# Performance work log

Measured on AMD Instinct MI355X. Metric: run time of the kernel, lower is better.

Reference implementation:

```python
import jax, jax.numpy as jnp
import numpy as np

H = 16  # num_heads (from init_kwargs)


def setup_inputs() -> dict:
    key = jax.random.key(0)
    ks = jax.random.split(key, 12)
    B, S, E = 4, 1024, 1024
    inp = {
        "query": jax.random.normal(ks[0], (B, S, E), jnp.float32),
        "key": jax.random.normal(ks[1], (B, S, E), jnp.float32),
        "value": jax.random.normal(ks[2], (B, S, E), jnp.float32),
        "mask": jax.random.randint(ks[3], (B, S, S), 0, 2, jnp.int32),
        # nn.Linear params: y = x @ W.T + b
        "Wq": jax.random.normal(ks[4], (E, E), jnp.float32) * 0.02,
        "bq": jnp.zeros((E,), jnp.float32),
        "Wk": jax.random.normal(ks[5], (E, E), jnp.float32) * 0.02,
        "bk": jnp.zeros((E,), jnp.float32),
        "Wv": jax.random.normal(ks[6], (E, E), jnp.float32) * 0.02,
        "bv": jnp.zeros((E,), jnp.float32),
        "Wo": jax.random.normal(ks[7], (E, E), jnp.float32) * 0.02,
        "bo": jnp.zeros((E,), jnp.float32),
    }
    return inp


def reference(query, key, value, mask, Wq, bq, Wk, bk, Wv, bv, Wo, bo):
    # Dropout treated as identity (eval mode) for a deterministic baseline.
    B, Sq, E = query.shape
    Sk = key.shape[1]
    D = E // H
    scale = jnp.sqrt(jnp.float32(D))

    Q = (query @ Wq.T + bq).reshape(B, Sq, H, D).transpose(0, 2, 1, 3)  # bhqd
    K = (key @ Wk.T + bk).reshape(B, Sk, H, D).transpose(0, 2, 1, 3)    # bhkd
    V = (value @ Wv.T + bv).reshape(B, Sk, H, D).transpose(0, 2, 1, 3)  # bhkd

    scores = jnp.einsum("bhqd,bhkd->bhqk", Q, K) / scale
    scores = jnp.where(mask[:, None, :, :] == 0, jnp.float32(-1e9), scores)
    attn = jax.nn.softmax(scores, axis=-1)  # [B,H,Sq,Sk]

    ctx = jnp.einsum("bhqk,bhkd->bhqd", attn, V)
    ctx = ctx.transpose(0, 2, 1, 3).reshape(B, Sq, E)
    out = ctx @ Wo.T + bo
    attn_avg = attn.mean(axis=1)  # [B,Sq,Sk]
    return out, attn_avg
```

## Files before the change

kernel.cpp:

```cpp
#include <hip/hip_runtime.h>
#include <hip/hip_bf16.h>
#include <stdint.h>

#define BATCH 4
#define SEQ   1024
#define EMB   1024
#define NH    16
#define HD    64

typedef short s8v __attribute__((ext_vector_type(8)));
typedef float f4v __attribute__((ext_vector_type(4)));

__device__ __forceinline__ uint16_t f2bf(float f) {
    __hip_bfloat16 h = __float2bfloat16(f);
    return *reinterpret_cast<uint16_t*>(&h);
}
__device__ __forceinline__ short bfraw(float f) {
    __hip_bfloat16 h = __float2bfloat16(f);
    return *reinterpret_cast<short*>(&h);
}
__device__ __forceinline__ s8v cvt8(const float* p) {
    float4 a = *(const float4*)p;
    float4 b = *(const float4*)(p + 4);
    s8v r;
    r[0] = bfraw(a.x); r[1] = bfraw(a.y); r[2] = bfraw(a.z); r[3] = bfraw(a.w);
    r[4] = bfraw(b.x); r[5] = bfraw(b.y); r[6] = bfraw(b.z); r[7] = bfraw(b.w);
    return r;
}

__global__ __launch_bounds__(256) void pack_mask(
        const int* __restrict__ mask, unsigned long long* __restrict__ Mb64)
{
    const size_t gid = (size_t)blockIdx.x * 256 + threadIdx.x;
    const unsigned long long bal = __ballot(mask[gid] != 0);
    if ((threadIdx.x & 63) == 0) Mb64[gid >> 6] = bal;
}

__global__ __launch_bounds__(256) void cvt_all(
        const float* __restrict__ W0, const float* __restrict__ W1,
        const float* __restrict__ W2, const float* __restrict__ W3,
        const float* __restrict__ X0, const float* __restrict__ X1,
        const float* __restrict__ X2,
        uint16_t* __restrict__ Wdst, uint16_t* __restrict__ Xq,
        uint16_t* __restrict__ Xk, uint16_t* __restrict__ Xv)
{
    const int y = blockIdx.y;
    const size_t off = ((size_t)blockIdx.x * 256 + threadIdx.x) * 8;
    if (y < 4) {
        if (blockIdx.x >= 512) return;
        const float* s = (y == 0) ? W0 : (y == 1) ? W1 : (y == 2) ? W2 : W3;
        *(s8v*)(Wdst + (size_t)y * EMB * EMB + off) = cvt8(s + off);
    } else {
        const float* s = (y == 4) ? X0 : (y == 5) ? X1 : X2;
        uint16_t*    d = (y == 4) ? Xq : (y == 5) ? Xk : Xv;
        *(s8v*)(d + off) = cvt8(s + off);
    }
}

__global__ __launch_bounds__(512, 2) void gemm3(
        const uint16_t* __restrict__ X0, const uint16_t* __restrict__ W0,
        const float* __restrict__ b0, void* __restrict__ o0, int sc0, float ss0,
        const uint16_t* __restrict__ X1, const uint16_t* __restrict__ W1,
        const float* __restrict__ b1, void* __restrict__ o1, int sc1, float ss1,
        const uint16_t* __restrict__ X2, const uint16_t* __restrict__ W2,
        const float* __restrict__ b2, void* __restrict__ o2, int sc2, float ss2)
{
    __shared__ __attribute__((aligned(16))) uint16_t As[2][128][40];
    __shared__ __attribute__((aligned(16))) uint16_t Bs[2][128][40];

    const int z = blockIdx.z;
    const uint16_t* Xb   = (z == 0) ? X0 : (z == 1) ? X1 : X2;
    const uint16_t* Wb   = (z == 0) ? W0 : (z == 1) ? W1 : W2;
    const float*    bias = (z == 0) ? b0 : (z == 1) ? b1 : b2;
    void*           outv = (z == 0) ? o0 : (z == 1) ? o1 : o2;
    const int     scatter = (z == 0) ? sc0 : (z == 1) ? sc1 : sc2;
    const float   scale   = (z == 0) ? ss0 : (z == 1) ? ss1 : ss2;

    const int t    = threadIdx.x;
    const int lane = t & 63;
    const int w    = t >> 6;
    const int wm = w & 1;
    const int wn = w >> 1;
    const int m0 = blockIdx.y * 128;
    const int n0 = blockIdx.x * 128;
    const int ar = lane & 15;
    const int aq = lane >> 4;

    const int srow = t >> 2;
    const int scol = (t & 3) * 8;

    const uint16_t* gA = Xb + (size_t)(m0 + srow) * EMB + scol;
    const uint16_t* gB = Wb + (size_t)(n0 + srow) * EMB + scol;

    f4v acc[4][2];
    #pragma unroll
    for (int i = 0; i < 4; ++i)
        #pragma unroll
        for (int j = 0; j < 2; ++j) acc[i][j] = (f4v){0.f, 0.f, 0.f, 0.f};

    s8v ra = *(const s8v*)gA;
    s8v rb = *(const s8v*)gB;

    for (int ki = 0; ki < 32; ++ki) {
        const int cur = ki & 1;
        *(s8v*)&As[cur][srow][scol] = ra;
        *(s8v*)&Bs[cur][srow][scol] = rb;
        __syncthreads();

        if (ki + 1 < 32) {
            const int kn = (ki + 1) * 32;
            ra = *(const s8v*)(gA + kn);
            rb = *(const s8v*)(gB + kn);
        }
        __builtin_amdgcn_sched_barrier(0);

        s8v af[4], bf[2];
        #pragma unroll
        for (int i = 0; i < 4; ++i)
            af[i] = *(const s8v*)&As[cur][wm * 64 + i * 16 + ar][aq * 8];
        #pragma unroll
        for (int j = 0; j < 2; ++j)
            bf[j] = *(const s8v*)&Bs[cur][wn * 32 + j * 16 + ar][aq * 8];
        #pragma unroll
        for (int i = 0; i < 4; ++i)
            #pragma unroll
            for (int j = 0; j < 2; ++j)
                acc[i][j] = __builtin_amdgcn_mfma_f32_16x16x32_bf16(af[i], bf[j], acc[i][j], 0, 0, 0);
    }

    #pragma unroll
    for (int i = 0; i < 4; ++i) {
        const int crow = m0 + wm * 64 + i * 16 + aq * 4;
        #pragma unroll
        for (int j = 0; j < 2; ++j) {
            const int n = n0 + wn * 32 + j * 16 + ar;
            const float bv = bias[n];
            #pragma unroll
            for (int r = 0; r < 4; ++r) {
                const int m = crow + r;
                const float v = (acc[i][j][r] + bv) * scale;
                if (scatter == 1) {
                    size_t idx = (size_t)(((m >> 10) * NH + (n >> 6)) * SEQ + (m & 1023)) * HD + (n & 63);
                    ((uint16_t*)outv)[idx] = f2bf(v);
                } else if (scatter == 2) {
                    size_t idx = (size_t)(((m >> 10) * NH + (n >> 6)) * HD + (n & 63)) * SEQ + (m & 1023);
                    ((uint16_t*)outv)[idx] = f2bf(v);
                } else {
                    ((float*)outv)[(size_t)m * EMB + n] = v;
                }
            }
        }
    }
}

__global__ __launch_bounds__(256, 4) void flash_ctx(
        const uint16_t* __restrict__ Qb, const uint16_t* __restrict__ Kb,
        const uint16_t* __restrict__ Vt, const uint32_t* __restrict__ Mb,
        uint16_t* __restrict__ ctx, float* __restrict__ linv_out)
{
    __shared__ uint32_t Ml[4][16][33];
    __shared__ __attribute__((aligned(16))) uint16_t Pt[4][2][16][56];

    const int t = threadIdx.x;
    const int w = t >> 6, lane = t & 63;
    const int ar = lane & 15, aq = lane >> 4;

    const int id   = blockIdx.x;
    const int xcd  = id & 7;
    const int rest = id >> 3;
    const int bh   = xcd * 8 + (rest & 7);
    const int qt   = (rest >> 3) * 4 + w;
    const int b = bh >> 4, h = bh & 15;
    const size_t hb = ((size_t)(b * NH + h)) * SEQ * HD;

    {
        const uint32_t* src = Mb + (((size_t)b * SEQ + qt * 16) << 5);
        uint4 m0 = *(const uint4*)(src + lane * 8);
        uint4 m1 = *(const uint4*)(src + lane * 8 + 4);
        const int pr = (lane * 8) >> 5, pc = (lane * 8) & 31;
        Ml[w][pr][pc + 0] = m0.x; Ml[w][pr][pc + 1] = m0.y;
        Ml[w][pr][pc + 2] = m0.z; Ml[w][pr][pc + 3] = m0.w;
        Ml[w][pr][pc + 4] = m1.x; Ml[w][pr][pc + 5] = m1.y;
        Ml[w][pr][pc + 6] = m1.z; Ml[w][pr][pc + 7] = m1.w;
    }

    const uint16_t* qp = Qb + hb + (size_t)(qt * 16 + ar) * HD + aq * 8;
    const s8v a0 = *(const s8v*)qp;
    const s8v a1 = *(const s8v*)(qp + 32);

    const uint16_t* kbase = Kb + hb + (size_t)ar * HD + aq * 8;
    const uint16_t* vbase = Vt + hb + (size_t)ar * SEQ + aq * 8;

    f4v OA0 = {0.f,0.f,0.f,0.f}, OA1 = OA0, OA2 = OA0, OA3 = OA0;
    f4v OB0 = OA0, OB1 = OA0, OB2 = OA0, OB3 = OA0;
    float lsA[4] = {0.f, 0.f, 0.f, 0.f};
    float lsB[4] = {0.f, 0.f, 0.f, 0.f};

    for (int ci = 0; ci < 16; ++ci) {
        const int cA = ci * 2, cB = ci * 2 + 1;
        const int kcA = cA * 32, kcB = cB * 32;

        const uint16_t* kA = kbase + (size_t)kcA * HD;
        const uint16_t* kB = kbase + (size_t)kcB * HD;
        s8v Abl0 = *(const s8v*)kA,            Abh0 = *(const s8v*)(kA + 32);
        s8v Abl1 = *(const s8v*)(kA + 16*HD),  Abh1 = *(const s8v*)(kA + 16*HD + 32);
        s8v Bbl0 = *(const s8v*)kB,            Bbh0 = *(const s8v*)(kB + 32);
        s8v Bbl1 = *(const s8v*)(kB + 16*HD),  Bbh1 = *(const s8v*)(kB + 16*HD + 32);

        f4v z = {0.f,0.f,0.f,0.f};
        f4v sA0 = __builtin_amdgcn_mfma_f32_16x16x32_bf16(a0, Abl0, z, 0, 0, 0);
        sA0 = __builtin_amdgcn_mfma_f32_16x16x32_bf16(a1, Abh0, sA0, 0, 0, 0);
        f4v sA1 = __builtin_amdgcn_mfma_f32_16x16x32_bf16(a0, Abl1, z, 0, 0, 0);
        sA1 = __builtin_amdgcn_mfma_f32_16x16x32_bf16(a1, Abh1, sA1, 0, 0, 0);
        f4v sB0 = __builtin_amdgcn_mfma_f32_16x16x32_bf16(a0, Bbl0, z, 0, 0, 0);
        sB0 = __builtin_amdgcn_mfma_f32_16x16x32_bf16(a1, Bbh0, sB0, 0, 0, 0);
        f4v sB1 = __builtin_amdgcn_mfma_f32_16x16x32_bf16(a0, Bbl1, z, 0, 0, 0);
        sB1 = __builtin_amdgcn_mfma_f32_16x16x32_bf16(a1, Bbh1, sB1, 0, 0, 0);

        const uint16_t* vA = vbase + kcA;
        const uint16_t* vB = vbase + kcB;
        s8v Av0 = *(const s8v*)(vA);
        s8v Av1 = *(const s8v*)(vA + 16 * SEQ);
        s8v Av2 = *(const s8v*)(vA + 32 * SEQ);
        s8v Av3 = *(const s8v*)(vA + 48 * SEQ);
        s8v Bv0 = *(const s8v*)(vB);
        s8v Bv1 = *(const s8v*)(vB + 16 * SEQ);
        s8v Bv2 = *(const s8v*)(vB + 32 * SEQ);
        s8v Bv3 = *(const s8v*)(vB + 48 * SEQ);

        #pragma unroll
        for (int r = 0; r < 4; ++r) {
            const uint32_t mwA = Ml[w][aq * 4 + r][cA];
            const float e0 = ((mwA >> ar) & 1u)        ? __expf(sA0[r]) : 0.f;
            const float e1 = ((mwA >> (16 + ar)) & 1u) ? __expf(sA1[r]) : 0.f;
            lsA[r] += e0 + e1;
            Pt[w][0][aq * 4 + r][ar]      = f2bf(e0);
            Pt[w][0][aq * 4 + r][16 + ar] = f2bf(e1);
        }
        #pragma unroll
        for (int r = 0; r < 4; ++r) {
            const uint32_t mwB = Ml[w][aq * 4 + r][cB];
            const float e0 = ((mwB >> ar) & 1u)        ? __expf(sB0[r]) : 0.f;
            const float e1 = ((mwB >> (16 + ar)) & 1u) ? __expf(sB1[r]) : 0.f;
            lsB[r] += e0 + e1;
            Pt[w][1][aq * 4 + r][ar]      = f2bf(e0);
            Pt[w][1][aq * 4 + r][16 + ar] = f2bf(e1);
        }

        const s8v paA = *(const s8v*)&Pt[w][0][ar][aq * 8];
        OA0 = __builtin_amdgcn_mfma_f32_16x16x32_bf16(paA, Av0, OA0, 0, 0, 0);
        OA1 = __builtin_amdgcn_mfma_f32_16x16x32_bf16(paA, Av1, OA1, 0, 0, 0);
        OA2 = __builtin_amdgcn_mfma_f32_16x16x32_bf16(paA, Av2, OA2, 0, 0, 0);
        OA3 = __builtin_amdgcn_mfma_f32_16x16x32_bf16(paA, Av3, OA3, 0, 0, 0);
        const s8v paB = *(const s8v*)&Pt[w][1][ar][aq * 8];
        OB0 = __builtin_amdgcn_mfma_f32_16x16x32_bf16(paB, Bv0, OB0, 0, 0, 0);
        OB1 = __builtin_amdgcn_mfma_f32_16x16x32_bf16(paB, Bv1, OB1, 0, 0, 0);
        OB2 = __builtin_amdgcn_mfma_f32_16x16x32_bf16(paB, Bv2, OB2, 0, 0, 0);
        OB3 = __builtin_amdgcn_mfma_f32_16x16x32_bf16(paB, Bv3, OB3, 0, 0, 0);
    }

    float lsum[4];
    #pragma unroll
    for (int r = 0; r < 4; ++r) {
        OA0[r] += OB0[r]; OA1[r] += OB1[r];
        OA2[r] += OB2[r]; OA3[r] += OB3[r];
        lsum[r] = lsA[r] + lsB[r];
    }

    #pragma unroll
    for (int off = 1; off < 16; off <<= 1) {
        #pragma unroll
        for (int r = 0; r < 4; ++r) lsum[r] += __shfl_xor(lsum[r], off);
    }
    float inv[4];
    #pragma unroll
    for (int r = 0; r < 4; ++r) inv[r] = 1.0f / lsum[r];

    #pragma unroll
    for (int r = 0; r < 4; ++r) {
        const int q = qt * 16 + aq * 4 + r;
        uint16_t* cp = ctx + ((size_t)(b * SEQ + q) * NH + h) * HD + ar;
        cp[ 0] = f2bf(OA0[r] * inv[r]);
        cp[16] = f2bf(OA1[r] * inv[r]);
        cp[32] = f2bf(OA2[r] * inv[r]);
        cp[48] = f2bf(OA3[r] * inv[r]);
    }
    if (ar == 0) {
        #pragma unroll
        for (int r = 0; r < 4; ++r)
            linv_out[(size_t)(b * NH + h) * SEQ + qt * 16 + aq * 4 + r] = inv[r];
    }
}

__global__ __launch_bounds__(512, 4) void attn_avg(
        const uint16_t* __restrict__ Qb, const uint16_t* __restrict__ Kb,
        const uint32_t* __restrict__ Mb, const float* __restrict__ linv,
        float* __restrict__ attn_out)
{
    const int qt = blockIdx.x;
    const int b  = blockIdx.y >> 2;
    const int kq = blockIdx.y & 3;
    const int t = threadIdx.x;
    const int w = t >> 6, lane = t & 63;
    const int ar = lane & 15, aq = lane >> 4;
    const int k0 = kq * 256 + w * 32;

    uint32_t mw[4];
    #pragma unroll
    for (int r = 0; r < 4; ++r)
        mw[r] = Mb[(((size_t)b * SEQ + qt * 16 + aq * 4 + r) << 5) + (k0 >> 5)];

    float acc[8];
    #pragma unroll
    for (int j = 0; j < 8; ++j) acc[j] = 0.f;

    for (int h = 0; h < NH; ++h) {
        const size_t hb = ((size_t)(b * NH + h)) * SEQ * HD;
        const uint16_t* qp = Qb + hb + (size_t)(qt * 16 + ar) * HD + aq * 8;
        const s8v a0 = *(const s8v*)qp;
        const s8v a1 = *(const s8v*)(qp + 32);
        float fs[4];
        #pragma unroll
        for (int r = 0; r < 4; ++r)
            fs[r] = linv[(size_t)(b * NH + h) * SEQ + qt * 16 + aq * 4 + r] * 0.0625f;

        #pragma unroll
        for (int nt = 0; nt < 2; ++nt) {
            const uint16_t* kp = Kb + hb + (size_t)(k0 + nt * 16 + ar) * HD + aq * 8;
            s8v bl = *(const s8v*)kp, bh2 = *(const s8v*)(kp + 32);
            f4v z = {0.f,0.f,0.f,0.f};
            f4v s = __builtin_amdgcn_mfma_f32_16x16x32_bf16(a0, bl, z, 0, 0, 0);
            s = __builtin_amdgcn_mfma_f32_16x16x32_bf16(a1, bh2, s, 0, 0, 0);
            #pragma unroll
            for (int r = 0; r < 4; ++r) {
                const int bit = nt * 16 + ar;
                if ((mw[r] >> bit) & 1u) acc[r * 2 + nt] += __expf(s[r]) * fs[r];
            }
        }
    }

    #pragma unroll
    for (int r = 0; r < 4; ++r) {
        float* ap = attn_out + ((size_t)b * SEQ + qt * 16 + aq * 4 + r) * SEQ + k0 + ar;
        #pragma unroll
        for (int nt = 0; nt < 2; ++nt) ap[nt * 16] = acc[r * 2 + nt];
    }
}

extern "C" void kernel_launch(void* const* d_in, const int* in_sizes, int n_in,
                              void* d_out, int out_size, void* d_ws, size_t ws_size,
                              hipStream_t stream) {
    const float* q_in = (const float*)d_in[0];
    const float* k_in = (const float*)d_in[1];
    const float* v_in = (const float*)d_in[2];
    const int*   mask = (const int*)d_in[3];
    const float* Wq = (const float*)d_in[4];
    const float* bq = (const float*)d_in[5];
    const float* Wk = (const float*)d_in[6];
    const float* bk = (const float*)d_in[7];
    const float* Wv = (const float*)d_in[8];
    const float* bv = (const float*)d_in[9];
    const float* Wo = (const float*)d_in[10];
    const float* bo = (const float*)d_in[11];

    float* out      = (float*)d_out;
    float* attn_out = out + (size_t)BATCH * SEQ * EMB;

    const size_t qkv_elems = (size_t)BATCH * NH * SEQ * HD;
    uint16_t* Qb  = (uint16_t*)d_ws;
    uint16_t* Kb  = Qb + qkv_elems;
    uint16_t* Vt  = Kb + qkv_elems;
    uint16_t* ctx = Vt + qkv_elems;
    uint16_t* Wcb = ctx + (size_t)BATCH * SEQ * EMB;
    uint16_t* Wqb = Wcb;
    uint16_t* Wkb = Wcb + (size_t)EMB * EMB;
    uint16_t* Wvb = Wcb + 2 * (size_t)EMB * EMB;
    uint16_t* Wob = Wcb + 3 * (size_t)EMB * EMB;
    uint16_t* Xq  = Wcb + 4 * (size_t)EMB * EMB;
    uint16_t* Xk  = Xq + qkv_elems;
    uint16_t* Xv  = ctx;
    uint32_t* Mb32 = (uint32_t*)(Xk + qkv_elems);
    float*    linv = (float*)(Mb32 + (size_t)BATCH * SEQ * 32);

    pack_mask<<<dim3((BATCH * SEQ * SEQ) / 256), 256, 0, stream>>>(
        mask, (unsigned long long*)Mb32);
    cvt_all<<<dim3(2048, 7), 256, 0, stream>>>(Wq, Wk, Wv, Wo, q_in, k_in, v_in,
                                               Wcb, Xq, Xk, Xv);

    dim3 g3(EMB / 128, (BATCH * SEQ) / 128, 3);
    gemm3<<<g3, 512, 0, stream>>>(
        Xq, Wqb, bq, Qb, 1, 0.125f,
        Xk, Wkb, bk, Kb, 1, 1.0f,
        Xv, Wvb, bv, Vt, 2, 1.0f);

    flash_ctx<<<dim3(1024), 256, 0, stream>>>(Qb, Kb, Vt, Mb32, ctx, linv);
    attn_avg<<<dim3(SEQ / 16, BATCH * 4), 512, 0, stream>>>(Qb, Kb, Mb32, linv, attn_out);

    dim3 g1(EMB / 128, (BATCH * SEQ) / 128, 1);
    gemm3<<<g1, 512, 0, stream>>>(
        ctx, Wob, bo, out, 0, 1.0f,
        ctx, Wob, bo, out, 0, 1.0f,
        ctx, Wob, bo, out, 0, 1.0f);
}
```

Measured before the change: 407.1 us.

## Use direct global-to-LDS loads with XOR swizzle and 4-wave GEMM tiles

Rewrites the projection GEMM so tiles are loaded straight into shared memory with global_load_lds instead of staging through registers. The LDS layout drops padding for an XOR-swizzled 32-element row to avoid bank conflicts. The block shrinks to 256 threads, with each wave computing a 64x64 sub-tile (16 MFMA accumulators). This cuts register staging and LDS store instructions, but raises per-wave register pressure and gives fewer waves per block for latency hiding. The correctness of the swizzle mapping for the LDS-direct load layout is a risk.

```diff
diff --git a/kernel.cpp b/kernel.cpp
--- a/kernel.cpp
+++ b/kernel.cpp
@@ -26,6 +26,11 @@
     r[0] = bfraw(a.x); r[1] = bfraw(a.y); r[2] = bfraw(a.z); r[3] = bfraw(a.w);
     r[4] = bfraw(b.x); r[5] = bfraw(b.y); r[6] = bfraw(b.z); r[7] = bfraw(b.w);
     return r;
+}
+__device__ __forceinline__ void gld16(const uint16_t* g, uint16_t* l) {
+    __builtin_amdgcn_global_load_lds(
+        (const __attribute__((address_space(1))) void*)g,
+        (__attribute__((address_space(3))) void*)l, 16, 0, 0);
 }
 
 __global__ __launch_bounds__(256) void pack_mask(
@@ -57,7 +62,7 @@
     }
 }
 
-__global__ __launch_bounds__(512, 2) void gemm3(
+__global__ __launch_bounds__(256) void gemm3(
         const uint16_t* __restrict__ X0, const uint16_t* __restrict__ W0,
         const float* __restrict__ b0, void* __restrict__ o0, int sc0, float ss0,
         const uint16_t* __restrict__ X1, const uint16_t* __restrict__ W1,
@@ -65,8 +70,8 @@
         const uint16_t* __restrict__ X2, const uint16_t* __restrict__ W2,
         const float* __restrict__ b2, void* __restrict__ o2, int sc2, float ss2)
 {
-    __shared__ __attribute__((aligned(16))) uint16_t As[2][128][40];
-    __shared__ __attribute__((aligned(16))) uint16_t Bs[2][128][40];
+    __shared__ __attribute__((aligned(16))) uint16_t As[2][128 * 32];
+    __shared__ __attribute__((aligned(16))) uint16_t Bs[2][128 * 32];
 
     const int z = blockIdx.z;
     const uint16_t* Xb   = (z == 0) ? X0 : (z == 1) ? X1 : X2;
@@ -86,45 +91,47 @@
     const int ar = lane & 15;
     const int aq = lane >> 4;
 
-    const int srow = t >> 2;
-    const int scol = (t & 3) * 8;
-
-    const uint16_t* gA = Xb + (size_t)(m0 + srow) * EMB + scol;
-    const uint16_t* gB = Wb + (size_t)(n0 + srow) * EMB + scol;
-
-    f4v acc[4][2];
+    const int srow = w * 32 + (lane >> 2);
+    const int scol = ((lane & 3) ^ ((lane >> 3) & 3)) * 8;
+    const uint16_t* gA0 = Xb + (size_t)(m0 + srow) * EMB + scol;
+    const uint16_t* gA1 = gA0 + (size_t)16 * EMB;
+    const uint16_t* gB0 = Wb + (size_t)(n0 + srow) * EMB + scol;
+    const uint16_t* gB1 = gB0 + (size_t)16 * EMB;
+    const int lb0 = w * 1024;
+    const int lb1 = lb0 + 512;
+
+    f4v acc[4][4];
     #pragma unroll
     for (int i = 0; i < 4; ++i)
         #pragma unroll
-        for (int j = 0; j < 2; ++j) acc[i][j] = (f4v){0.f, 0.f, 0.f, 0.f};
-
-    s8v ra = *(const s8v*)gA;
-    s8v rb = *(const s8v*)gB;
+        for (int j = 0; j < 4; ++j) acc[i][j] = (f4v){0.f, 0.f, 0.f, 0.f};
+
+    gld16(gA0, &As[0][lb0]); gld16(gA1, &As[0][lb1]);
+    gld16(gB0, &Bs[0][lb0]); gld16(gB1, &Bs[0][lb1]);
+
+    const int sl = (aq ^ ((ar >> 1) & 3)) * 8;
 
     for (int ki = 0; ki < 32; ++ki) {
-        const int cur = ki & 1;
-        *(s8v*)&As[cur][srow][scol] = ra;
-        *(s8v*)&Bs[cur][srow][scol] = rb;
         __syncthreads();
-
         if (ki + 1 < 32) {
             const int kn = (ki + 1) * 32;
-            ra = *(const s8v*)(gA + kn);
-            rb = *(const s8v*)(gB + kn);
+            const int nb = (ki + 1) & 1;
+            gld16(gA0 + kn, &As[nb][lb0]); gld16(gA1 + kn, &As[nb][lb1]);
+            gld16(gB0 + kn, &Bs[nb][lb0]); gld16(gB1 + kn, &Bs[nb][lb1]);
         }
-        __builtin_amdgcn_sched_barrier(0);
-
-        s8v af[4], bf[2];
+        const uint16_t* Ab = &As[ki & 1][0];
+        const uint16_t* Bb = &Bs[ki & 1][0];
+        s8v af[4], bf[4];
         #pragma unroll
         for (int i = 0; i < 4; ++i)
-            af[i] = *(const s8v*)&As[cur][wm * 64 + i * 16 + ar][aq * 8];
-        #pragma unroll
-        for (int j = 0; j < 2; ++j)
-            bf[j] = *(const s8v*)&Bs[cur][wn * 32 + j * 16 + ar][aq * 8];
+            af[i] = *(const s8v*)(Ab + (wm * 64 + i * 16 + ar) * 32 + sl);
+        #pragma unroll
+        for (int j = 0; j < 4; ++j)
+            bf[j] = *(const s8v*)(Bb + (wn * 64 + j * 16 + ar) * 32 + sl);
         #pragma unroll
         for (int i = 0; i < 4; ++i)
             #pragma unroll
-            for (int j = 0; j < 2; ++j)
+            for (int j = 0; j < 4; ++j)
                 acc[i][j] = __builtin_amdgcn_mfma_f32_16x16x32_bf16(af[i], bf[j], acc[i][j], 0, 0, 0);
     }
 
@@ -132,8 +139,8 @@
     for (int i = 0; i < 4; ++i) {
         const int crow = m0 + wm * 64 + i * 16 + aq * 4;
         #pragma unroll
-        for (int j = 0; j < 2; ++j) {
-            const int n = n0 + wn * 32 + j * 16 + ar;
+        for (int j = 0; j < 4; ++j) {
+            const int n = n0 + wn * 64 + j * 16 + ar;
             const float bv = bias[n];
             #pragma unroll
             for (int r = 0; r < 4; ++r) {
@@ -388,7 +395,7 @@
                                                Wcb, Xq, Xk, Xv);
 
     dim3 g3(EMB / 128, (BATCH * SEQ) / 128, 3);
-    gemm3<<<g3, 512, 0, stream>>>(
+    gemm3<<<g3, 256, 0, stream>>>(
         Xq, Wqb, bq, Qb, 1, 0.125f,
         Xk, Wkb, bk, Kb, 1, 1.0f,
         Xv, Wvb, bv, Vt, 2, 1.0f);
@@ -397,7 +404,7 @@
     attn_avg<<<dim3(SEQ / 16, BATCH * 4), 512, 0, stream>>>(Qb, Kb, Mb32, linv, attn_out);
 
     dim3 g1(EMB / 128, (BATCH * SEQ) / 128, 1);
-    gemm3<<<g1, 512, 0, stream>>>(
+    gemm3<<<g1, 256, 0, stream>>>(
         ctx, Wob, bo, out, 0, 1.0f,
         ctx, Wob, bo, out, 0, 1.0f,
         ctx, Wob, bo, out, 0, 1.0f);
```

Measured after the change: 420.7 us. 3.3% more time.
